# Performance work log

Measured on AMD Instinct MI355X. Metric: run time of the kernel, lower is better.

Reference implementation:

```python
import jax, jax.numpy as jnp
import numpy as np

N = 100_000   # nodes
D = 128       # emb_size
E = 1_600_000 # edges (avg degree 16)
K = 64        # K1 (channel 0 pooling clusters)
LAYERS = 2


def _l2norm(x):
    # F.normalize(x, dim=-1, p=2) with eps=1e-12
    return x / jnp.maximum(jnp.linalg.norm(x, axis=-1, keepdims=True), 1e-12)


def setup_inputs() -> dict:
    key = jax.random.key(0)
    ks = jax.random.split(key, 9)
    return {
        "adj": jax.random.uniform(ks[0], (N,), dtype=jnp.float32),
        "edge_row": jax.random.randint(ks[1], (E,), 0, N),
        "edge_col": jax.random.randint(ks[2], (E,), 0, N),
        "edge_val": jax.random.uniform(ks[3], (E,), dtype=jnp.float32),
        "embedding": jax.random.normal(ks[4], (N, D), dtype=jnp.float32) * 0.02,
        "W_item0": jax.random.normal(ks[5], (D, D), dtype=jnp.float32) * 0.05,
        "W_item1": jax.random.normal(ks[6], (D, D), dtype=jnp.float32) * 0.05,
        "W_i1": jax.random.normal(ks[7], (D, D), dtype=jnp.float32) * 0.05,
        "W_i2": jax.random.normal(ks[8], (D, K), dtype=jnp.float32) * 0.05,
        "channel": 0,
    }


def reference(adj, edge_row, edge_col, edge_val, embedding,
              W_item0, W_item1, W_i1, W_i2, channel):
    n = adj.shape[0]

    def spmm(x):  # sparse [N,N] @ dense [N,D] via COO gather + segment_sum
        return jax.ops.segment_sum(edge_val[:, None] * x[edge_col], edge_row,
                                   num_segments=n)

    x = embedding
    final = [x]
    finalh = []
    for W in (W_item0, W_item1):  # structurally distinct per-layer weights
        x = spmm(x @ W)                                   # [N,D]
        H1 = jax.nn.relu(x @ W_i1 + x)                    # [N,D]
        H1 = jax.nn.softmax(H1 @ W_i2, axis=1)            # [N,K]
        h = H1.T * adj                                    # [K,N]
        h = h * (1.0 / (jnp.sum(h, axis=0) + 1e-8))       # column-normalize
        h = H1 @ (h @ x)                                  # [N,K]@[K,D] -> [N,D]
        x = h + x
        final.append(_l2norm(x))
        finalh.append(_l2norm(h))
    item_embeddings = sum(final) / (LAYERS + 1)
    hs = sum(finalh) / LAYERS
    return item_embeddings, hs
```

## Files before the change

kernel.cpp:

```cpp
#include <hip/hip_runtime.h>

constexpr int DD = 128;
constexpr int KK = 64;
constexpr int NBLK_C2 = 512;
constexpr int CH = 512;

typedef __attribute__((ext_vector_type(8))) short bf16x8;
typedef __attribute__((ext_vector_type(4))) float f32x4;

union U4 { unsigned u[4]; int4 i4; bf16x8 v; };

__device__ inline unsigned bf16_rne(float x) {
  unsigned u = __float_as_uint(x);
  u += 0x7fff + ((u >> 16) & 1);
  return u >> 16;
}
__device__ inline float bf16f(unsigned h) { return __uint_as_float(h << 16); }
__device__ inline void split2(float a, float b, unsigned& hi, unsigned& lo) {
  const unsigned h0 = bf16_rne(a), h1 = bf16_rne(b);
  const unsigned l0 = bf16_rne(a - bf16f(h0)), l1 = bf16_rne(b - bf16f(h1));
  hi = h0 | (h1 << 16);
  lo = l0 | (l1 << 16);
}

__global__ void k_prepW(const float* __restrict__ W, unsigned* __restrict__ Whi,
                        unsigned* __restrict__ Wlo) {
  const int id = blockIdx.x * 256 + threadIdx.x;
  const int j = id & 3, l = (id >> 2) & 63, t = (id >> 8) & 7, ks = id >> 11;
  const int k0 = 32 * ks + 8 * (l >> 4) + 2 * j;
  const int col = 16 * t + (l & 15);
  const float e0 = W[k0 * 128 + col], e1 = W[(k0 + 1) * 128 + col];
  unsigned hi, lo;
  split2(e0, e1, hi, lo);
  Whi[id] = hi;
  Wlo[id] = lo;
}

__global__ void k_prepWs(const float* __restrict__ W, unsigned* __restrict__ Wf) {
  const int id = blockIdx.x * 256 + threadIdx.x;
  const int j = id & 3, l = (id >> 2) & 63, t = (id >> 8) & 3, ks = id >> 10;
  const int k0 = 32 * ks + 8 * (l >> 4) + 2 * j;
  const int col = 16 * t + (l & 15);
  const unsigned h0 = bf16_rne(W[k0 * 64 + col]);
  const unsigned h1 = bf16_rne(W[(k0 + 1) * 64 + col]);
  Wf[id] = h0 | (h1 << 16);
}

__global__ __launch_bounds__(512) void k_gemm_mfma(const float* __restrict__ X,
                                                   const unsigned* __restrict__ Whi,
                                                   const unsigned* __restrict__ Wlo,
                                                   unsigned short* __restrict__ Yb,
                                                   int n) {
  __shared__ unsigned sb[2 * 8192];
  {
    const int t = threadIdx.x;
    uint4* d0 = (uint4*)sb;
    const uint4* s0 = (const uint4*)Whi;
#pragma unroll
    for (int i = 0; i < 4; ++i) d0[t + 512 * i] = s0[t + 512 * i];
    uint4* d1 = (uint4*)(sb + 8192);
    const uint4* s1 = (const uint4*)Wlo;
#pragma unroll
    for (int i = 0; i < 4; ++i) d1[t + 512 * i] = s1[t + 512 * i];
  }
  __syncthreads();
  const int wave = threadIdx.x >> 6, lane = threadIdx.x & 63;
  const int l15 = lane & 15, lhi = lane >> 4;
  const int row0 = blockIdx.x * 256 + wave * 32;
  if (row0 >= n) return;
  f32x4 acc[2][8];
#pragma unroll
  for (int rt = 0; rt < 2; ++rt)
#pragma unroll
    for (int t = 0; t < 8; ++t) acc[rt][t] = (f32x4){0.f, 0.f, 0.f, 0.f};
#pragma unroll
  for (int ks = 0; ks < 4; ++ks) {
    U4 ah[2], al[2];
#pragma unroll
    for (int rt = 0; rt < 2; ++rt) {
      int r = row0 + rt * 16 + l15;
      if (r >= n) r = n - 1;
      const float4 x0 = *(const float4*)&X[(size_t)r * DD + ks * 32 + lhi * 8];
      const float4 x1 = *(const float4*)&X[(size_t)r * DD + ks * 32 + lhi * 8 + 4];
      split2(x0.x, x0.y, ah[rt].u[0], al[rt].u[0]);
      split2(x0.z, x0.w, ah[rt].u[1], al[rt].u[1]);
      split2(x1.x, x1.y, ah[rt].u[2], al[rt].u[2]);
      split2(x1.z, x1.w, ah[rt].u[3], al[rt].u[3]);
    }
#pragma unroll
    for (int t = 0; t < 8; ++t) {
      U4 bh, bl;
      const int off = ((ks * 8 + t) * 64 + lane) * 4;
      bh.i4 = *(const int4*)&sb[off];
      bl.i4 = *(const int4*)&sb[8192 + off];
#pragma unroll
      for (int rt = 0; rt < 2; ++rt) {
        acc[rt][t] = __builtin_amdgcn_mfma_f32_16x16x32_bf16(ah[rt].v, bh.v, acc[rt][t], 0, 0, 0);
        acc[rt][t] = __builtin_amdgcn_mfma_f32_16x16x32_bf16(al[rt].v, bh.v, acc[rt][t], 0, 0, 0);
        acc[rt][t] = __builtin_amdgcn_mfma_f32_16x16x32_bf16(ah[rt].v, bl.v, acc[rt][t], 0, 0, 0);
      }
    }
  }
#pragma unroll
  for (int rt = 0; rt < 2; ++rt)
#pragma unroll
    for (int rr = 0; rr < 4; ++rr) {
      const int row = row0 + rt * 16 + lhi * 4 + rr;
      if (row < n) {
#pragma unroll
        for (int t = 0; t < 8; ++t)
          Yb[(size_t)row * DD + t * 16 + l15] =
              (unsigned short)bf16_rne(acc[rt][t][rr]);
      }
    }
}

__global__ void k_hist(const int* __restrict__ er, int* __restrict__ cnt, int E) {
  for (long e = (long)blockIdx.x * blockDim.x + threadIdx.x; e < E;
       e += (long)gridDim.x * blockDim.x)
    atomicAdd(&cnt[er[e]], 1);
}

__global__ __launch_bounds__(256) void k_chunksum(const int* __restrict__ cnt,
                                                  int* __restrict__ csum, int n) {
  const int c = blockIdx.x, t = threadIdx.x;
  const int i0 = c * CH + 2 * t;
  int s2 = 0;
  if (i0 < n) s2 += cnt[i0];
  if (i0 + 1 < n) s2 += cnt[i0 + 1];
#pragma unroll
  for (int off = 32; off >= 1; off >>= 1) s2 += __shfl_xor(s2, off);
  __shared__ int ws_[4];
  if ((t & 63) == 0) ws_[t >> 6] = s2;
  __syncthreads();
  if (t == 0) csum[c] = ws_[0] + ws_[1] + ws_[2] + ws_[3];
}

__global__ __launch_bounds__(256) void k_chunkscan(const int* __restrict__ csum,
                                                   int* __restrict__ coff, int nch) {
  __shared__ int s[256];
  const int t = threadIdx.x;
  const int v = (t < nch) ? csum[t] : 0;
  s[t] = v;
  __syncthreads();
  for (int off = 1; off < 256; off <<= 1) {
    const int u = (t >= off) ? s[t - off] : 0;
    __syncthreads();
    s[t] += u;
    __syncthreads();
  }
  coff[t] = s[t] - v;
}

__global__ __launch_bounds__(256) void k_rowptr(const int* __restrict__ cnt,
                                                const int* __restrict__ coff,
                                                int* __restrict__ rowptr,
                                                int n, int E) {
  const int c = blockIdx.x, t = threadIdx.x;
  const int i0 = c * CH + 2 * t, i1 = i0 + 1;
  const int v0 = (i0 < n) ? cnt[i0] : 0;
  const int v1 = (i1 < n) ? cnt[i1] : 0;
  __shared__ int s[256];
  const int s2 = v0 + v1;
  s[t] = s2;
  __syncthreads();
  for (int off = 1; off < 256; off <<= 1) {
    const int u = (t >= off) ? s[t - off] : 0;
    __syncthreads();
    s[t] += u;
    __syncthreads();
  }
  const int excl = s[t] - s2 + coff[c];
  if (i0 < n) rowptr[i0] = excl;
  if (i1 < n) rowptr[i1] = excl + v0;
  if (c == 0 && t == 0) rowptr[n] = E;
}

__global__ void k_scatter(const int* __restrict__ er, const int* __restrict__ ec,
                          const float* __restrict__ ev,
                          const int* __restrict__ rowptr, int* __restrict__ cur,
                          int2* __restrict__ erec, int E) {
  for (long e = (long)blockIdx.x * blockDim.x + threadIdx.x; e < E;
       e += (long)gridDim.x * blockDim.x) {
    const int r = er[e];
    const int pos = rowptr[r] + atomicAdd(&cur[r], 1);
    erec[pos] = make_int2(ec[e], __float_as_int(ev[e]));
  }
}

__global__ __launch_bounds__(256) void k_spmm_csr(const int* __restrict__ rowptr,
                                                  const int2* __restrict__ erec,
                                                  const unsigned* __restrict__ Yb,
                                                  float* __restrict__ Xo, int n) {
  const int lane = threadIdx.x & 63;
  const int c0 = 2 * lane;
  const long gw = (long)blockIdx.x * 4 + (threadIdx.x >> 6);
  const long nw = (long)gridDim.x * 4;
  for (long row = gw; row < n; row += nw) {
    const int b = rowptr[row], e2 = rowptr[row + 1];
    float a0 = 0.f, a1 = 0.f, b0 = 0.f, b1 = 0.f;
    float c00 = 0.f, c1 = 0.f, d0 = 0.f, d1 = 0.f;
    int e = b;
    for (; e + 4 <= e2; e += 4) {
      const int2 r0 = erec[e], r1 = erec[e + 1];
      const int2 r2 = erec[e + 2], r3 = erec[e + 3];
      const unsigned q0 = Yb[(size_t)r0.x * (DD / 2) + lane];
      const unsigned q1 = Yb[(size_t)r1.x * (DD / 2) + lane];
      const unsigned q2 = Yb[(size_t)r2.x * (DD / 2) + lane];
      const unsigned q3 = Yb[(size_t)r3.x * (DD / 2) + lane];
      const float v0 = __int_as_float(r0.y), v1 = __int_as_float(r1.y);
      const float v2 = __int_as_float(r2.y), v3 = __int_as_float(r3.y);
      a0 = fmaf(v0, __uint_as_float(q0 << 16), a0);
      a1 = fmaf(v0, __uint_as_float(q0 & 0xffff0000u), a1);
      b0 = fmaf(v1, __uint_as_float(q1 << 16), b0);
      b1 = fmaf(v1, __uint_as_float(q1 & 0xffff0000u), b1);
      c00 = fmaf(v2, __uint_as_float(q2 << 16), c00);
      c1 = fmaf(v2, __uint_as_float(q2 & 0xffff0000u), c1);
      d0 = fmaf(v3, __uint_as_float(q3 << 16), d0);
      d1 = fmaf(v3, __uint_as_float(q3 & 0xffff0000u), d1);
    }
    for (; e + 2 <= e2; e += 2) {
      const int2 r0 = erec[e], r1 = erec[e + 1];
      const float v0 = __int_as_float(r0.y), v1 = __int_as_float(r1.y);
      const unsigned q0 = Yb[(size_t)r0.x * (DD / 2) + lane];
      const unsigned q1 = Yb[(size_t)r1.x * (DD / 2) + lane];
      a0 = fmaf(v0, __uint_as_float(q0 << 16), a0);
      a1 = fmaf(v0, __uint_as_float(q0 & 0xffff0000u), a1);
      b0 = fmaf(v1, __uint_as_float(q1 << 16), b0);
      b1 = fmaf(v1, __uint_as_float(q1 & 0xffff0000u), b1);
    }
    if (e < e2) {
      const int2 r0 = erec[e];
      const float v = __int_as_float(r0.y);
      const unsigned q = Yb[(size_t)r0.x * (DD / 2) + lane];
      a0 = fmaf(v, __uint_as_float(q << 16), a0);
      a1 = fmaf(v, __uint_as_float(q & 0xffff0000u), a1);
    }
    *(float2*)&Xo[(size_t)row * DD + c0] =
        make_float2((a0 + b0) + (c00 + d0), (a1 + b1) + (c1 + d1));
  }
}

__global__ __launch_bounds__(512) void k_c1_mfma(const float* __restrict__ X,
                                                 const unsigned* __restrict__ W1hi,
                                                 const unsigned* __restrict__ W1lo,
                                                 const unsigned* __restrict__ W2f,
                                                 const float* __restrict__ adj,
                                                 float* __restrict__ H1g,
                                                 float* __restrict__ trow, int n) {
  __shared__ unsigned s1[2 * 8192];
  __shared__ unsigned s2[4096];
  __shared__ unsigned h1s[8 * 16 * 68];
  {
    const int t = threadIdx.x;
    uint4* d0 = (uint4*)s1;
    const uint4* sA = (const uint4*)W1hi;
    const uint4* sB = (const uint4*)W1lo;
#pragma unroll
    for (int i = 0; i < 4; ++i) d0[t + 512 * i] = sA[t + 512 * i];
    uint4* d1 = (uint4*)(s1 + 8192);
#pragma unroll
    for (int i = 0; i < 4; ++i) d1[t + 512 * i] = sB[t + 512 * i];
    uint4* d2 = (uint4*)s2;
    const uint4* sC = (const uint4*)W2f;
#pragma unroll
    for (int i = 0; i < 2; ++i) d2[t + 512 * i] = sC[t + 512 * i];
  }
  __syncthreads();
  const int wave = threadIdx.x >> 6, lane = threadIdx.x & 63;
  const int l15 = lane & 15, lhi = lane >> 4;
  unsigned* __restrict__ h1w = h1s + wave * (16 * 68);
  const int row0 = blockIdx.x * 128 + wave * 16;
  if (row0 >= n) return;

  U4 ah[4], al[4];
#pragma unroll
  for (int ks = 0; ks < 4; ++ks) {
    int r = row0 + l15;
    if (r >= n) r = n - 1;
    const float4 x0 = *(const float4*)&X[(size_t)r * DD + ks * 32 + lhi * 8];
    const float4 x1 = *(const float4*)&X[(size_t)r * DD + ks * 32 + lhi * 8 + 4];
    split2(x0.x, x0.y, ah[ks].u[0], al[ks].u[0]);
    split2(x0.z, x0.w, ah[ks].u[1], al[ks].u[1]);
    split2(x1.x, x1.y, ah[ks].u[2], al[ks].u[2]);
    split2(x1.z, x1.w, ah[ks].u[3], al[ks].u[3]);
  }
  f32x4 acc1[8];
#pragma unroll
  for (int t = 0; t < 8; ++t) acc1[t] = (f32x4){0.f, 0.f, 0.f, 0.f};
#pragma unroll
  for (int ks = 0; ks < 4; ++ks) {
#pragma unroll
    for (int t = 0; t < 8; ++t) {
      U4 bh, bl;
      const int off = ((ks * 8 + t) * 64 + lane) * 4;
      bh.i4 = *(const int4*)&s1[off];
      bl.i4 = *(const int4*)&s1[8192 + off];
      acc1[t] = __builtin_amdgcn_mfma_f32_16x16x32_bf16(ah[ks].v, bh.v, acc1[t], 0, 0, 0);
      acc1[t] = __builtin_amdgcn_mfma_f32_16x16x32_bf16(al[ks].v, bh.v, acc1[t], 0, 0, 0);
      acc1[t] = __builtin_amdgcn_mfma_f32_16x16x32_bf16(ah[ks].v, bl.v, acc1[t], 0, 0, 0);
    }
  }

  unsigned short* __restrict__ h16 = (unsigned short*)h1w;
#pragma unroll
  for (int rr = 0; rr < 4; ++rr) {
    int row = row0 + 4 * lhi + rr;
    if (row >= n) row = n - 1;
    const float* __restrict__ xr = X + (size_t)row * DD;
#pragma unroll
    for (int t = 0; t < 8; ++t) {
      float v = acc1[t][rr] + xr[16 * t + l15];
      v = fmaxf(v, 0.f);
      h16[(4 * lhi + rr) * 136 + 16 * t + l15] = (unsigned short)bf16_rne(v);
    }
  }

  f32x4 acc3[4];
#pragma unroll
  for (int t = 0; t < 4; ++t) acc3[t] = (f32x4){0.f, 0.f, 0.f, 0.f};
#pragma unroll
  for (int ks = 0; ks < 4; ++ks) {
    U4 a3;
    a3.i4 = *(const int4*)&h1w[l15 * 68 + ks * 16 + lhi * 4];
#pragma unroll
    for (int t = 0; t < 4; ++t) {
      U4 b3;
      b3.i4 = *(const int4*)&s2[((ks * 4 + t) * 64 + lane) * 4];
      acc3[t] = __builtin_amdgcn_mfma_f32_16x16x32_bf16(a3.v, b3.v, acc3[t], 0, 0, 0);
    }
  }

#pragma unroll
  for (int rr = 0; rr < 4; ++rr) {
    const int row = row0 + 4 * lhi + rr;
    float z0 = acc3[0][rr], z1 = acc3[1][rr], z2 = acc3[2][rr], z3 = acc3[3][rr];
    float m = fmaxf(fmaxf(z0, z1), fmaxf(z2, z3));
#pragma unroll
    for (int off = 8; off >= 1; off >>= 1) m = fmaxf(m, __shfl_xor(m, off));
    const float p0 = expf(z0 - m), p1 = expf(z1 - m);
    const float p2 = expf(z2 - m), p3 = expf(z3 - m);
    float s = p0 + p1 + p2 + p3;
#pragma unroll
    for (int off = 8; off >= 1; off >>= 1) s += __shfl_xor(s, off);
    const float inv = 1.0f / s;
    if (row < n) {
      float* __restrict__ hr = H1g + (size_t)row * KK;
      hr[l15] = p0 * inv;
      hr[16 + l15] = p1 * inv;
      hr[32 + l15] = p2 * inv;
      hr[48 + l15] = p3 * inv;
      if (l15 == 0) {
        const float a = adj[row];
        trow[row] = a / (a + 1e-8f);
      }
    }
  }
}

__global__ __launch_bounds__(1024, 4) void k_c2(const float* __restrict__ X,
                                                const float* __restrict__ trow,
                                                const float* __restrict__ H1g,
                                                float* __restrict__ Mpart, int n) {
  __shared__ float cmb[3 * 4 * 16 * 2 * 64];
  const int t = threadIdx.x;
  const int wave = t >> 6, lane = t & 63;
  const int rg = wave >> 2, kg = wave & 3;
  const int kb = kg * 16;
  const int d0 = 2 * lane;
  float macc[16][2];
#pragma unroll
  for (int j = 0; j < 16; ++j) { macc[j][0] = 0.f; macc[j][1] = 0.f; }
  const int bx = blockIdx.x;
  for (long row = (long)bx + 512L * rg; row < n; row += 2048L) {
    const int r = __builtin_amdgcn_readfirstlane((int)row);
    const float tr = trow[r];
    const float2 xv = *(const float2*)&X[(size_t)r * DD + d0];
    const float px0 = tr * xv.x, px1 = tr * xv.y;
    const float* __restrict__ hrow = H1g + (size_t)r * KK + kb;
#pragma unroll
    for (int j = 0; j < 16; ++j) {
      const float hj = hrow[j];
      macc[j][0] = fmaf(hj, px0, macc[j][0]);
      macc[j][1] = fmaf(hj, px1, macc[j][1]);
    }
  }
  if (rg > 0) {
    float* __restrict__ dst = cmb + ((rg - 1) * 4 + kg) * (16 * 2 * 64);
#pragma unroll
    for (int j = 0; j < 16; ++j) {
      dst[(2 * j + 0) * 64 + lane] = macc[j][0];
      dst[(2 * j + 1) * 64 + lane] = macc[j][1];
    }
  }
  __syncthreads();
  if (rg == 0) {
#pragma unroll
    for (int g = 0; g < 3; ++g) {
      const float* __restrict__ src = cmb + (g * 4 + kg) * (16 * 2 * 64);
#pragma unroll
      for (int j = 0; j < 16; ++j) {
        macc[j][0] += src[(2 * j + 0) * 64 + lane];
        macc[j][1] += src[(2 * j + 1) * 64 + lane];
      }
    }
    float* __restrict__ mp = Mpart + (size_t)bx * (KK * DD);
#pragma unroll
    for (int j = 0; j < 16; ++j)
      *(float2*)&mp[(kb + j) * DD + d0] = make_float2(macc[j][0], macc[j][1]);
  }
}

__global__ void k_dred1(const float* __restrict__ Mpart, float* __restrict__ Mp2) {
  const int j = blockIdx.x * blockDim.x + threadIdx.x;
  const int i = j & (KK * DD - 1);
  const int c = j >> 13;
  float s = 0.f;
#pragma unroll
  for (int q = 0; q < 16; ++q)
    s += Mpart[(size_t)(c * 16 + q) * (KK * DD) + i];
  Mp2[(size_t)c * (KK * DD) + i] = s;
}

__global__ void k_dred2(const float* __restrict__ Mp2, float* __restrict__ Mg) {
  const int i = blockIdx.x * blockDim.x + threadIdx.x;
  float s = 0.f;
#pragma unroll
  for (int c = 0; c < 32; ++c) s += Mp2[(size_t)c * (KK * DD) + i];
  Mg[i] = s;
}

__global__ __launch_bounds__(256) void k_fin(const float* __restrict__ H1g,
                                             const float* __restrict__ Mg,
                                             const float* __restrict__ emb,
                                             float* __restrict__ Xb,
                                             float* __restrict__ out,
                                             int n, int first) {
  __shared__ float Ml[KK * DD];
  for (int i = threadIdx.x; i < KK * DD / 4; i += 256)
    ((float4*)Ml)[i] = ((const float4*)Mg)[i];
  __syncthreads();
  const int wave = threadIdx.x >> 6, lane = threadIdx.x & 63;
  const int c0 = 2 * lane;
  const size_t hoff = (size_t)n * DD;
  const long nw = (long)gridDim.x * 4;
  for (long g = (long)blockIdx.x * 4 + wave; g * 4 < n; g += nw) {
    const int row0 = (int)(g * 4);
    const int r0u = __builtin_amdgcn_readfirstlane(row0);
    int nr = n - r0u; if (nr > 4) nr = 4;
    int rb[4];
#pragma unroll
    for (int r = 0; r < 4; ++r) rb[r] = (r < nr ? r : 0) * KK;
    const float* __restrict__ hp = H1g + (size_t)r0u * KK;
    float a0[4], a1[4];
#pragma unroll
    for (int r = 0; r < 4; ++r) { a0[r] = 0.f; a1[r] = 0.f; }
#pragma unroll 2
    for (int k = 0; k < KK; k += 4) {
      const float2 mv0 = *(const float2*)&Ml[(k + 0) * DD + c0];
      const float2 mv1 = *(const float2*)&Ml[(k + 1) * DD + c0];
      const float2 mv2 = *(const float2*)&Ml[(k + 2) * DD + c0];
      const float2 mv3 = *(const float2*)&Ml[(k + 3) * DD + c0];
#pragma unroll
      for (int r = 0; r < 4; ++r) {
        const float4 hq = *(const float4*)&hp[rb[r] + k];
        a0[r] = fmaf(hq.x, mv0.x, a0[r]); a1[r] = fmaf(hq.x, mv0.y, a1[r]);
        a0[r] = fmaf(hq.y, mv1.x, a0[r]); a1[r] = fmaf(hq.y, mv1.y, a1[r]);
        a0[r] = fmaf(hq.z, mv2.x, a0[r]); a1[r] = fmaf(hq.z, mv2.y, a1[r]);
        a0[r] = fmaf(hq.w, mv3.x, a0[r]); a1[r] = fmaf(hq.w, mv3.y, a1[r]);
      }
    }
#pragma unroll
    for (int r = 0; r < 4; ++r) {
      if (r >= nr) break;
      const int row = row0 + r;
      const float2 xv = *(const float2*)&Xb[(size_t)row * DD + c0];
      const float h0 = a0[r], h1 = a1[r];
      const float x0 = h0 + xv.x, x1 = h1 + xv.y;
      float sh = h0 * h0 + h1 * h1;
      float sx = x0 * x0 + x1 * x1;
#pragma unroll
      for (int off = 32; off >= 1; off >>= 1) {
        sh += __shfl_xor(sh, off);
        sx += __shfl_xor(sx, off);
      }
      const float ih = 0.5f / fmaxf(sqrtf(sh), 1e-12f);
      const float ix = (1.0f / 3.0f) / fmaxf(sqrtf(sx), 1e-12f);
      *(float2*)&Xb[(size_t)row * DD + c0] = make_float2(x0, x1);
      const size_t oi = (size_t)row * DD + c0;
      float2 ci, ch;
      if (first) {
        ci.x = emb[oi] * (1.0f / 3.0f); ci.y = emb[oi + 1] * (1.0f / 3.0f);
        ch.x = 0.f; ch.y = 0.f;
      } else {
        ci = *(const float2*)&out[oi];
        ch = *(const float2*)&out[hoff + oi];
      }
      ci.x += x0 * ix; ci.y += x1 * ix;
      ch.x += h0 * ih; ch.y += h1 * ih;
      *(float2*)&out[oi] = ci;
      *(float2*)&out[hoff + oi] = ch;
    }
  }
}

extern "C" void kernel_launch(void* const* d_in, const int* in_sizes, int n_in,
                              void* d_out, int out_size, void* d_ws, size_t ws_size,
                              hipStream_t stream) {
  const float* adj  = (const float*)d_in[0];
  const int*   erow = (const int*)d_in[1];
  const int*   ecol = (const int*)d_in[2];
  const float* eval = (const float*)d_in[3];
  const float* emb  = (const float*)d_in[4];
  const float* W0   = (const float*)d_in[5];
  const float* W1   = (const float*)d_in[6];
  const float* Wi1  = (const float*)d_in[7];
  const float* Wi2  = (const float*)d_in[8];
  const int n = in_sizes[0];
  const int E = in_sizes[1];
  float* out = (float*)d_out;

  float* xb    = (float*)d_ws;
  float* yb    = xb + (size_t)n * DD;
  unsigned short* Ybf = (unsigned short*)yb;
  float* H1g   = yb + (size_t)n * (DD / 2);
  float* Mpart = H1g + (size_t)n * KK;
  float* Mp2   = Mpart + (size_t)NBLK_C2 * KK * DD;
  float* Mg    = Mp2 + (size_t)32 * KK * DD;
  int*   cnt    = (int*)(Mg + KK * DD);
  int*   rowptr = cnt + n;
  int*   csum   = rowptr + n + 4;
  int*   coff   = csum + 256;
  int2*  erec   = (int2*)(coff + 256);
  float* trow   = (float*)(erec + E);
  unsigned* w0hi  = (unsigned*)(trow + n);
  unsigned* w0lo  = w0hi + 8192;
  unsigned* w1hi_ = w0lo + 8192;
  unsigned* w1lo_ = w1hi_ + 8192;
  unsigned* wi1hi = w1lo_ + 8192;
  unsigned* wi1lo = wi1hi + 8192;
  unsigned* wi2f  = wi1lo + 8192;

  const int NCH = (n + CH - 1) / CH;

  k_prepW<<<32, 256, 0, stream>>>(W0, w0hi, w0lo);
  k_prepW<<<32, 256, 0, stream>>>(W1, w1hi_, w1lo_);
  k_prepW<<<32, 256, 0, stream>>>(Wi1, wi1hi, wi1lo);
  k_prepWs<<<16, 256, 0, stream>>>(Wi2, wi2f);

  hipMemsetAsync(cnt, 0, (size_t)n * sizeof(int), stream);
  k_hist<<<2048, 256, 0, stream>>>(erow, cnt, E);
  k_chunksum<<<NCH, 256, 0, stream>>>(cnt, csum, n);
  k_chunkscan<<<1, 256, 0, stream>>>(csum, coff, NCH);
  k_rowptr<<<NCH, 256, 0, stream>>>(cnt, coff, rowptr, n, E);
  hipMemsetAsync(cnt, 0, (size_t)n * sizeof(int), stream);
  k_scatter<<<2048, 256, 0, stream>>>(erow, ecol, eval, rowptr, cnt, erec, E);

  const int g_gm  = (n + 255) / 256;
  const int g_c1m = (n + 127) / 128;

  for (int L = 0; L < 2; ++L) {
    const unsigned* Whi = (L == 0) ? w0hi : w1hi_;
    const unsigned* Wlo = (L == 0) ? w0lo : w1lo_;
    const float* Xin = (L == 0) ? emb : xb;
    k_gemm_mfma<<<g_gm, 512, 0, stream>>>(Xin, Whi, Wlo, Ybf, n);
    k_spmm_csr<<<2048, 256, 0, stream>>>(rowptr, erec, (const unsigned*)Ybf, xb, n);
    k_c1_mfma<<<g_c1m, 512, 0, stream>>>(xb, wi1hi, wi1lo, wi2f, adj, H1g, trow, n);
    k_c2<<<NBLK_C2, 1024, 0, stream>>>(xb, trow, H1g, Mpart, n);
    k_dred1<<<1024, 256, 0, stream>>>(Mpart, Mp2);
    k_dred2<<<32, 256, 0, stream>>>(Mp2, Mg);
    k_fin<<<1280, 256, 0, stream>>>(H1g, Mg, emb, xb, out, n, (L == 0) ? 1 : 0);
  }
}
```

Measured before the change: 734.0 us.

## Use split-bf16 MFMA for final H1@M product and partition edge scatter by row range

The final per-layer product H1 @ (h@x) moves from scalar FMA with an LDS-resident M to bf16 MFMA, using a hi/lo split (three MFMAs per tile) to keep near-fp32 accuracy. A new small kernel packs M into the MFMA fragment layout each layer. Separately, the CSR scatter now has each block read one edge slice and handle only rows in one of eight row ranges, so atomics and writes land in a narrower address window at the cost of reading each edge eight times. The fused normalization and output accumulation now use a 16-lane column layout with narrower stores.

```diff
diff --git a/kernel.cpp b/kernel.cpp
--- a/kernel.cpp
+++ b/kernel.cpp
@@ -44,6 +44,18 @@
   const unsigned h0 = bf16_rne(W[k0 * 64 + col]);
   const unsigned h1 = bf16_rne(W[(k0 + 1) * 64 + col]);
   Wf[id] = h0 | (h1 << 16);
+}
+
+__global__ void k_prepM(const float* __restrict__ M, unsigned* __restrict__ Mhi,
+                        unsigned* __restrict__ Mlo) {
+  const int id = blockIdx.x * 256 + threadIdx.x;
+  const int j = id & 3, l = (id >> 2) & 63, t = (id >> 8) & 7, ks = id >> 11;
+  const int k0 = 32 * ks + 8 * (l >> 4) + 2 * j;
+  const int col = 16 * t + (l & 15);
+  unsigned hi, lo;
+  split2(M[k0 * 128 + col], M[(k0 + 1) * 128 + col], hi, lo);
+  Mhi[id] = hi;
+  Mlo[id] = lo;
 }
 
 __global__ __launch_bounds__(512) void k_gemm_mfma(const float* __restrict__ X,
@@ -179,12 +191,19 @@
 __global__ void k_scatter(const int* __restrict__ er, const int* __restrict__ ec,
                           const float* __restrict__ ev,
                           const int* __restrict__ rowptr, int* __restrict__ cur,
-                          int2* __restrict__ erec, int E) {
-  for (long e = (long)blockIdx.x * blockDim.x + threadIdx.x; e < E;
-       e += (long)gridDim.x * blockDim.x) {
+                          int2* __restrict__ erec, int E, int n) {
+  const int rng = blockIdx.x & 7;
+  const int g = blockIdx.x >> 3;
+  const long e_lo = (long)g * E / 256;
+  const long e_hi = (long)(g + 1) * E / 256;
+  const int r_lo = (int)((long)rng * n / 8);
+  const int r_hi = (int)((long)(rng + 1) * n / 8);
+  for (long e = e_lo + threadIdx.x; e < e_hi; e += 256) {
     const int r = er[e];
-    const int pos = rowptr[r] + atomicAdd(&cur[r], 1);
-    erec[pos] = make_int2(ec[e], __float_as_int(ev[e]));
+    if (r >= r_lo && r < r_hi) {
+      const int pos = rowptr[r] + atomicAdd(&cur[r], 1);
+      erec[pos] = make_int2(ec[e], __float_as_int(ev[e]));
+    }
   }
 }
 
@@ -430,76 +449,100 @@
   Mg[i] = s;
 }
 
-__global__ __launch_bounds__(256) void k_fin(const float* __restrict__ H1g,
-                                             const float* __restrict__ Mg,
-                                             const float* __restrict__ emb,
-                                             float* __restrict__ Xb,
-                                             float* __restrict__ out,
-                                             int n, int first) {
-  __shared__ float Ml[KK * DD];
-  for (int i = threadIdx.x; i < KK * DD / 4; i += 256)
-    ((float4*)Ml)[i] = ((const float4*)Mg)[i];
+__global__ __launch_bounds__(512) void k_fin_mfma(const float* __restrict__ H1g,
+                                                  const unsigned* __restrict__ Mhi,
+                                                  const unsigned* __restrict__ Mlo,
+                                                  const float* __restrict__ emb,
+                                                  float* __restrict__ Xb,
+                                                  float* __restrict__ out,
+                                                  int n, int first) {
+  __shared__ unsigned sm[2 * 4096];
+  {
+    const int t = threadIdx.x;
+    uint4* d0 = (uint4*)sm;
+    const uint4* s0 = (const uint4*)Mhi;
+#pragma unroll
+    for (int i = 0; i < 2; ++i) d0[t + 512 * i] = s0[t + 512 * i];
+    uint4* d1 = (uint4*)(sm + 4096);
+    const uint4* s1 = (const uint4*)Mlo;
+#pragma unroll
+    for (int i = 0; i < 2; ++i) d1[t + 512 * i] = s1[t + 512 * i];
+  }
   __syncthreads();
   const int wave = threadIdx.x >> 6, lane = threadIdx.x & 63;
-  const int c0 = 2 * lane;
+  const int l15 = lane & 15, lhi = lane >> 4;
   const size_t hoff = (size_t)n * DD;
-  const long nw = (long)gridDim.x * 4;
-  for (long g = (long)blockIdx.x * 4 + wave; g * 4 < n; g += nw) {
-    const int row0 = (int)(g * 4);
-    const int r0u = __builtin_amdgcn_readfirstlane(row0);
-    int nr = n - r0u; if (nr > 4) nr = 4;
-    int rb[4];
-#pragma unroll
-    for (int r = 0; r < 4; ++r) rb[r] = (r < nr ? r : 0) * KK;
-    const float* __restrict__ hp = H1g + (size_t)r0u * KK;
-    float a0[4], a1[4];
-#pragma unroll
-    for (int r = 0; r < 4; ++r) { a0[r] = 0.f; a1[r] = 0.f; }
-#pragma unroll 2
-    for (int k = 0; k < KK; k += 4) {
-      const float2 mv0 = *(const float2*)&Ml[(k + 0) * DD + c0];
-      const float2 mv1 = *(const float2*)&Ml[(k + 1) * DD + c0];
-      const float2 mv2 = *(const float2*)&Ml[(k + 2) * DD + c0];
-      const float2 mv3 = *(const float2*)&Ml[(k + 3) * DD + c0];
-#pragma unroll
-      for (int r = 0; r < 4; ++r) {
-        const float4 hq = *(const float4*)&hp[rb[r] + k];
-        a0[r] = fmaf(hq.x, mv0.x, a0[r]); a1[r] = fmaf(hq.x, mv0.y, a1[r]);
-        a0[r] = fmaf(hq.y, mv1.x, a0[r]); a1[r] = fmaf(hq.y, mv1.y, a1[r]);
-        a0[r] = fmaf(hq.z, mv2.x, a0[r]); a1[r] = fmaf(hq.z, mv2.y, a1[r]);
-        a0[r] = fmaf(hq.w, mv3.x, a0[r]); a1[r] = fmaf(hq.w, mv3.y, a1[r]);
+  const int row0 = blockIdx.x * 128 + wave * 16;
+  if (row0 >= n) return;
+
+  U4 ah[2], al[2];
+  {
+    int ra = row0 + l15;
+    if (ra >= n) ra = n - 1;
+    const float* __restrict__ hp = H1g + (size_t)ra * KK;
+#pragma unroll
+    for (int ks = 0; ks < 2; ++ks) {
+      const float4 x0 = *(const float4*)&hp[ks * 32 + lhi * 8];
+      const float4 x1 = *(const float4*)&hp[ks * 32 + lhi * 8 + 4];
+      split2(x0.x, x0.y, ah[ks].u[0], al[ks].u[0]);
+      split2(x0.z, x0.w, ah[ks].u[1], al[ks].u[1]);
+      split2(x1.x, x1.y, ah[ks].u[2], al[ks].u[2]);
+      split2(x1.z, x1.w, ah[ks].u[3], al[ks].u[3]);
+    }
+  }
+  f32x4 acc[8];
+#pragma unroll
+  for (int t = 0; t < 8; ++t) acc[t] = (f32x4){0.f, 0.f, 0.f, 0.f};
+#pragma unroll
+  for (int ks = 0; ks < 2; ++ks) {
+#pragma unroll
+    for (int t = 0; t < 8; ++t) {
+      U4 bh, bl;
+      const int off = ((ks * 8 + t) * 64 + lane) * 4;
+      bh.i4 = *(const int4*)&sm[off];
+      bl.i4 = *(const int4*)&sm[4096 + off];
+      acc[t] = __builtin_amdgcn_mfma_f32_16x16x32_bf16(ah[ks].v, bh.v, acc[t], 0, 0, 0);
+      acc[t] = __builtin_amdgcn_mfma_f32_16x16x32_bf16(al[ks].v, bh.v, acc[t], 0, 0, 0);
+      acc[t] = __builtin_amdgcn_mfma_f32_16x16x32_bf16(ah[ks].v, bl.v, acc[t], 0, 0, 0);
+    }
+  }
+#pragma unroll
+  for (int rr = 0; rr < 4; ++rr) {
+    const int row = row0 + 4 * lhi + rr;
+    const int rc = (row < n) ? row : (n - 1);
+    float hh[8], xx[8];
+    float sh = 0.f, sx = 0.f;
+#pragma unroll
+    for (int t = 0; t < 8; ++t) {
+      const float xv = Xb[(size_t)rc * DD + 16 * t + l15];
+      hh[t] = acc[t][rr];
+      xx[t] = hh[t] + xv;
+      sh = fmaf(hh[t], hh[t], sh);
+      sx = fmaf(xx[t], xx[t], sx);
+    }
+#pragma unroll
+    for (int off = 8; off >= 1; off >>= 1) {
+      sh += __shfl_xor(sh, off);
+      sx += __shfl_xor(sx, off);
+    }
+    const float ih = 0.5f / fmaxf(sqrtf(sh), 1e-12f);
+    const float ix = (1.0f / 3.0f) / fmaxf(sqrtf(sx), 1e-12f);
+    if (row < n) {
+#pragma unroll
+      for (int t = 0; t < 8; ++t) {
+        const size_t oi = (size_t)row * DD + 16 * t + l15;
+        Xb[oi] = xx[t];
+        float ci, ch;
+        if (first) {
+          ci = emb[oi] * (1.0f / 3.0f);
+          ch = 0.f;
+        } else {
+          ci = out[oi];
+          ch = out[hoff + oi];
+        }
+        out[oi] = ci + xx[t] * ix;
+        out[hoff + oi] = ch + hh[t] * ih;
       }
-    }
-#pragma unroll
-    for (int r = 0; r < 4; ++r) {
-      if (r >= nr) break;
-      const int row = row0 + r;
-      const float2 xv = *(const float2*)&Xb[(size_t)row * DD + c0];
-      const float h0 = a0[r], h1 = a1[r];
-      const float x0 = h0 + xv.x, x1 = h1 + xv.y;
-      float sh = h0 * h0 + h1 * h1;
-      float sx = x0 * x0 + x1 * x1;
-#pragma unroll
-      for (int off = 32; off >= 1; off >>= 1) {
-        sh += __shfl_xor(sh, off);
-        sx += __shfl_xor(sx, off);
-      }
-      const float ih = 0.5f / fmaxf(sqrtf(sh), 1e-12f);
-      const float ix = (1.0f / 3.0f) / fmaxf(sqrtf(sx), 1e-12f);
-      *(float2*)&Xb[(size_t)row * DD + c0] = make_float2(x0, x1);
-      const size_t oi = (size_t)row * DD + c0;
-      float2 ci, ch;
-      if (first) {
-        ci.x = emb[oi] * (1.0f / 3.0f); ci.y = emb[oi + 1] * (1.0f / 3.0f);
-        ch.x = 0.f; ch.y = 0.f;
-      } else {
-        ci = *(const float2*)&out[oi];
-        ch = *(const float2*)&out[hoff + oi];
-      }
-      ci.x += x0 * ix; ci.y += x1 * ix;
-      ch.x += h0 * ih; ch.y += h1 * ih;
-      *(float2*)&out[oi] = ci;
-      *(float2*)&out[hoff + oi] = ch;
     }
   }
 }
@@ -540,6 +583,8 @@
   unsigned* wi1hi = w1lo_ + 8192;
   unsigned* wi1lo = wi1hi + 8192;
   unsigned* wi2f  = wi1lo + 8192;
+  unsigned* mhi   = wi2f + 4096;
+  unsigned* mlo   = mhi + 4096;
 
   const int NCH = (n + CH - 1) / CH;
 
@@ -554,10 +599,11 @@
   k_chunkscan<<<1, 256, 0, stream>>>(csum, coff, NCH);
   k_rowptr<<<NCH, 256, 0, stream>>>(cnt, coff, rowptr, n, E);
   hipMemsetAsync(cnt, 0, (size_t)n * sizeof(int), stream);
-  k_scatter<<<2048, 256, 0, stream>>>(erow, ecol, eval, rowptr, cnt, erec, E);
+  k_scatter<<<2048, 256, 0, stream>>>(erow, ecol, eval, rowptr, cnt, erec, E, n);
 
   const int g_gm  = (n + 255) / 256;
   const int g_c1m = (n + 127) / 128;
+  const int g_fin = (n + 127) / 128;
 
   for (int L = 0; L < 2; ++L) {
     const unsigned* Whi = (L == 0) ? w0hi : w1hi_;
@@ -569,6 +615,7 @@
     k_c2<<<NBLK_C2, 1024, 0, stream>>>(xb, trow, H1g, Mpart, n);
     k_dred1<<<1024, 256, 0, stream>>>(Mpart, Mp2);
     k_dred2<<<32, 256, 0, stream>>>(Mp2, Mg);
-    k_fin<<<1280, 256, 0, stream>>>(H1g, Mg, emb, xb, out, n, (L == 0) ? 1 : 0);
-  }
-}
+    k_prepM<<<16, 256, 0, stream>>>(Mg, mhi, mlo);
+    k_fin_mfma<<<g_fin, 512, 0, stream>>>(H1g, mhi, mlo, emb, xb, out, n, (L == 0) ? 1 : 0);
+  }
+}
```

Result: faster. 711.0 us (-3.1%).
